# Performance work log

Measured on AMD Instinct MI355X. Metric: run time of the kernel, lower is better.

Reference implementation:

```python
import jax, jax.numpy as jnp
import numpy as np

NEG_SLOPE = 0.2


def gat_conv(x, src, dst, W, a_src, a_dst, bias, heads, out_ch):
    """PyG-style GATConv (concat=True, self-loops already appended)."""
    N = x.shape[0]
    h = (x @ W).reshape(N, heads, out_ch)            # [N,H,C]
    al_s = jnp.einsum('nhc,hc->nh', h, a_src)        # [N,H]
    al_d = jnp.einsum('nhc,hc->nh', h, a_dst)        # [N,H]
    e = al_s[src] + al_d[dst]                        # [E,H]
    e = jnp.where(e > 0, e, NEG_SLOPE * e)           # leaky_relu
    # segment softmax over edges grouped by destination node
    m = jax.ops.segment_max(e, dst, num_segments=N)  # [N,H]
    ex = jnp.exp(e - m[dst])
    s = jax.ops.segment_sum(ex, dst, num_segments=N)
    alpha = ex / s[dst]                              # [E,H]
    msg = alpha[:, :, None] * h[src]                 # [E,H,C]
    out = jax.ops.segment_sum(msg, dst, num_segments=N)  # [N,H,C]
    return out.reshape(N, heads * out_ch) + bias


def setup_inputs() -> dict:
    key = jax.random.key(0)
    ks = jax.random.split(key, 10)
    N, E = 100000, 1600000
    return {
        'x': jax.random.normal(ks[0], (N, 4), dtype=jnp.float32),
        'edge_index': jax.random.randint(ks[1], (2, E), 0, N, dtype=jnp.int64),
        'W1': jax.random.normal(ks[2], (4, 32), dtype=jnp.float32) * 0.5,
        'a_src1': jax.random.normal(ks[3], (2, 16), dtype=jnp.float32) * 0.5,
        'a_dst1': jax.random.normal(ks[4], (2, 16), dtype=jnp.float32) * 0.5,
        'b1': jax.random.normal(ks[5], (32,), dtype=jnp.float32) * 0.1,
        'W2': jax.random.normal(ks[6], (32, 2), dtype=jnp.float32) * 0.2,
        'a_src2': jax.random.normal(ks[7], (1, 2), dtype=jnp.float32) * 0.5,
        'a_dst2': jax.random.normal(ks[8], (1, 2), dtype=jnp.float32) * 0.5,
        'b2': jax.random.normal(ks[9], (2,), dtype=jnp.float32) * 0.1,
    }


def reference(x, edge_index, W1, a_src1, a_dst1, b1, W2, a_src2, a_dst2, b2):
    N = x.shape[0]
    loop = jnp.arange(N, dtype=edge_index.dtype)     # add_self_loops=True
    src = jnp.concatenate([edge_index[0], loop])
    dst = jnp.concatenate([edge_index[1], loop])
    # dropout(p=0.6) is identity at inference
    h = gat_conv(x, src, dst, W1, a_src1, a_dst1, b1, heads=2, out_ch=16)
    h = jax.nn.elu(h)
    out = gat_conv(h, src, dst, W2, a_src2, a_dst2, b2, heads=1, out_ch=2)
    return out
```

## Files before the change

### kernel.cpp

```cpp
#include <hip/hip_runtime.h>
#include <math.h>

#define NEG_SLOPE 0.2f
#define SCAN_CHUNK 2048
#define ECLAMP 80.0f
#define BUCKET_SHIFT 8
#define BUCKET_MASK 255
#define EB_CHUNK 8192

__device__ __forceinline__ float lrelu(float e) {
    return e > 0.f ? e : NEG_SLOPE * e;
}

__global__ void k0_prep1(const float* __restrict__ x,
                         const float* __restrict__ W1,
                         const float* __restrict__ a_src1,
                         const float* __restrict__ a_dst1,
                         float* __restrict__ as1,
                         float* __restrict__ ad1,
                         int N) {
    int t = blockIdx.x * blockDim.x + threadIdx.x;
    int n = t >> 5;
    int c = t & 31;
    if (n >= N) return;
    const float4 xv = reinterpret_cast<const float4*>(x)[n];
    float h = xv.x * W1[c] + xv.y * W1[32 + c] + xv.z * W1[64 + c] + xv.w * W1[96 + c];
    float ts = h * a_src1[c];
    float td = h * a_dst1[c];
#pragma unroll
    for (int m = 8; m >= 1; m >>= 1) {
        ts += __shfl_xor(ts, m);
        td += __shfl_xor(td, m);
    }
    if ((c & 15) == 0) {
        int hh = c >> 4;
        as1[n * 2 + hh] = ts;
        ad1[n * 2 + hh] = td;
    }
}

__global__ void p1_hist(const int* __restrict__ dst, int* __restrict__ cmatT,
                        int E, int NB, int nblkE) {
    __shared__ int cnt[512];
    const int blk = blockIdx.x, tid = threadIdx.x;
    for (int b = tid; b < NB; b += 256) cnt[b] = 0;
    __syncthreads();
    int base = blk * EB_CHUNK;
    int end = min(base + EB_CHUNK, E);
    for (int e = base + tid; e < end; e += 256)
        atomicAdd(&cnt[dst[e] >> BUCKET_SHIFT], 1);
    __syncthreads();
    for (int b = tid; b < NB; b += 256)
        cmatT[(size_t)b * nblkE + blk] = cnt[b];
}

__global__ void k2a_partials(const int* __restrict__ in, int* __restrict__ bsum, int n) {
    __shared__ int ws[4];
    const int tid = threadIdx.x;
    const int lane = tid & 63, wid = tid >> 6;
    int base = blockIdx.x * SCAN_CHUNK + tid * 8;
    int lsum = 0;
#pragma unroll
    for (int i = 0; i < 8; ++i) {
        int idx = base + i;
        lsum += (idx < n) ? in[idx] : 0;
    }
#pragma unroll
    for (int m = 32; m >= 1; m >>= 1) lsum += __shfl_xor(lsum, m);
    if (lane == 0) ws[wid] = lsum;
    __syncthreads();
    if (tid == 0) bsum[blockIdx.x] = ws[0] + ws[1] + ws[2] + ws[3];
}

__global__ void k2b_scanb(const int* __restrict__ bsum, int* __restrict__ bscan, int nb) {
    __shared__ int wsum[16];
    const int tid = threadIdx.x;
    const int lane = tid & 63, wid = tid >> 6;
    int carry = 0;
    for (int base = 0; base < nb; base += 1024) {
        int i = base + tid;
        int v = (i < nb) ? bsum[i] : 0;
        int xx = v;
#pragma unroll
        for (int off = 1; off < 64; off <<= 1) {
            int t = __shfl_up(xx, off);
            if (lane >= off) xx += t;
        }
        if (lane == 63) wsum[wid] = xx;
        __syncthreads();
        int woff = 0;
        for (int w = 0; w < wid; ++w) woff += wsum[w];
        if (i < nb) bscan[i] = carry + woff + xx - v;
        int tot = 0;
        for (int w = 0; w < 16; ++w) tot += wsum[w];
        carry += tot;
        __syncthreads();
    }
}

__global__ void k2c_scan(const int* __restrict__ in, const int* __restrict__ bscan,
                         int* __restrict__ out, int n) {
    __shared__ int ws[4];
    const int tid = threadIdx.x;
    const int lane = tid & 63, wid = tid >> 6;
    int base = blockIdx.x * SCAN_CHUNK + tid * 8;
    int v[8], pre[8];
    int lsum = 0;
#pragma unroll
    for (int i = 0; i < 8; ++i) {
        int idx = base + i;
        v[i] = (idx < n) ? in[idx] : 0;
        pre[i] = lsum;
        lsum += v[i];
    }
    int xs = lsum;
#pragma unroll
    for (int off = 1; off < 64; off <<= 1) {
        int t = __shfl_up(xs, off);
        if (lane >= off) xs += t;
    }
    if (lane == 63) ws[wid] = xs;
    __syncthreads();
    int woff = 0;
    for (int w = 0; w < wid; ++w) woff += ws[w];
    int off0 = bscan[blockIdx.x] + woff + xs - lsum;
#pragma unroll
    for (int i = 0; i < 8; ++i) {
        int idx = base + i;
        if (idx < n) out[idx] = off0 + pre[i];
    }
}

__global__ void p3_scatter(const int* __restrict__ src, const int* __restrict__ dst,
                           const int* __restrict__ cscan, unsigned int* __restrict__ ebuf,
                           int E, int NB, int nblkE) {
    __shared__ int cur[512];
    const int blk = blockIdx.x, tid = threadIdx.x;
    for (int b = tid; b < NB; b += 256)
        cur[b] = cscan[(size_t)b * nblkE + blk];
    __syncthreads();
    int base = blk * EB_CHUNK;
    int end = min(base + EB_CHUNK, E);
    for (int e = base + tid; e < end; e += 256) {
        int d = dst[e];
        int b = d >> BUCKET_SHIFT;
        int pos = atomicAdd(&cur[b], 1);
        ebuf[pos] = (unsigned int)src[e] | ((unsigned int)(d & BUCKET_MASK) << 24);
    }
}

__global__ void p4_csr(const unsigned int* __restrict__ ebuf,
                       const int* __restrict__ cscan,
                       int* __restrict__ rp, int* __restrict__ esrt,
                       int N, int E, int NB, int nblkE) {
    __shared__ int degl[256];
    __shared__ int curl[256];
    __shared__ int wsum[4];
    const int b = blockIdx.x, tid = threadIdx.x;
    const int lane = tid & 63, wid = tid >> 6;
    int bstart = cscan[(size_t)b * nblkE];
    int bend = (b + 1 < NB) ? cscan[(size_t)(b + 1) * nblkE] : E;
    degl[tid] = 0;
    __syncthreads();
    for (int i = bstart + tid; i < bend; i += 256)
        atomicAdd(&degl[ebuf[i] >> 24], 1);
    __syncthreads();
    int v = degl[tid];
    int xs = v;
#pragma unroll
    for (int off = 1; off < 64; off <<= 1) {
        int t = __shfl_up(xs, off);
        if (lane >= off) xs += t;
    }
    if (lane == 63) wsum[wid] = xs;
    __syncthreads();
    int woff = 0;
    for (int w = 0; w < wid; ++w) woff += wsum[w];
    int excl = woff + xs - v;
    int node = (b << BUCKET_SHIFT) + tid;
    if (node < N) rp[node] = bstart + excl;
    curl[tid] = bstart + excl;
    if (b == 0 && tid == 0) rp[N] = E;
    __syncthreads();
    for (int i = bstart + tid; i < bend; i += 256) {
        unsigned int ev = ebuf[i];
        int dl = ev >> 24;
        int pos = atomicAdd(&curl[dl], 1);
        esrt[pos] = (int)(ev & 0x00FFFFFFu);
    }
}

__global__ void k4_layer1(const int* __restrict__ rp, const int* __restrict__ esrt,
                          const float* __restrict__ x, const float* __restrict__ as1,
                          const float* __restrict__ ad1, const float* __restrict__ b1,
                          const float* __restrict__ W1,
                          const float* __restrict__ W2, const float* __restrict__ a_src2,
                          const float* __restrict__ a_dst2,
                          float4* __restrict__ h2p, float* __restrict__ ad2,
                          int N) {
    int t = blockIdx.x * blockDim.x + threadIdx.x;
    int n = t >> 3;
    int l = t & 7;
    if (n >= N) return;
    int h = l >> 2;
    int d = l & 3;
    float ad = ad1[n * 2 + h];
    float es = lrelu(as1[n * 2 + h] + ad);
    float ws = __expf(fminf(es, ECLAMP));
    float g0 = ws * x[(size_t)n * 4 + d], g1 = 0.f, g2 = 0.f, g3 = 0.f;
    float s0 = ws, s1 = 0.f, s2 = 0.f, s3 = 0.f;

    int p0 = rp[n], p1 = rp[n + 1];
    int p = p0;
    for (; p + 3 < p1; p += 4) {
        int sa = esrt[p];
        int sb = esrt[p + 1];
        int sc_ = esrt[p + 2];
        int sd = esrt[p + 3];
        float ea = lrelu(as1[(size_t)sa * 2 + h] + ad);
        float eb = lrelu(as1[(size_t)sb * 2 + h] + ad);
        float ec = lrelu(as1[(size_t)sc_ * 2 + h] + ad);
        float ed = lrelu(as1[(size_t)sd * 2 + h] + ad);
        float xa = x[(size_t)sa * 4 + d];
        float xb = x[(size_t)sb * 4 + d];
        float xc = x[(size_t)sc_ * 4 + d];
        float xd = x[(size_t)sd * 4 + d];
        float wa = __expf(fminf(ea, ECLAMP));
        float wb = __expf(fminf(eb, ECLAMP));
        float wc = __expf(fminf(ec, ECLAMP));
        float wd = __expf(fminf(ed, ECLAMP));
        s0 += wa;  g0 += wa * xa;
        s1 += wb;  g1 += wb * xb;
        s2 += wc;  g2 += wc * xc;
        s3 += wd;  g3 += wd * xd;
    }
    for (; p < p1; ++p) {
        int sa = esrt[p];
        float ea = lrelu(as1[(size_t)sa * 2 + h] + ad);
        float xa = x[(size_t)sa * 4 + d];
        float wa = __expf(fminf(ea, ECLAMP));
        s0 += wa;  g0 += wa * xa;
    }
    float s = (s0 + s1) + (s2 + s3);
    float agg = ((g0 + g1) + (g2 + g3)) / s;

    float a2[2][4];
#pragma unroll
    for (int k = 0; k < 8; ++k)
        a2[k >> 2][k & 3] = __shfl(agg, k, 8);

    float t0 = 0.f, t1 = 0.f;
#pragma unroll
    for (int j = 0; j < 4; ++j) {
        int c = l * 4 + j;
        int hc = c >> 4;
        float o = b1[c]
                + a2[hc][0] * W1[c]
                + a2[hc][1] * W1[32 + c]
                + a2[hc][2] * W1[64 + c]
                + a2[hc][3] * W1[96 + c];
        o = o > 0.f ? o : expm1f(o);
        t0 += o * W2[c * 2 + 0];
        t1 += o * W2[c * 2 + 1];
    }
#pragma unroll
    for (int msk = 1; msk <= 4; msk <<= 1) {
        t0 += __shfl_xor(t0, msk);
        t1 += __shfl_xor(t1, msk);
    }
    if (l == 0) {
        float as2v = t0 * a_src2[0] + t1 * a_src2[1];
        float ad2v = t0 * a_dst2[0] + t1 * a_dst2[1];
        h2p[n] = make_float4(t0, t1, as2v, 0.f);
        ad2[n] = ad2v;
    }
}

__global__ void k5_layer2(const int* __restrict__ rp, const int* __restrict__ esrt,
                          const float4* __restrict__ h2p, const float* __restrict__ ad2,
                          const float* __restrict__ b2,
                          float* __restrict__ out, int N) {
    int t = blockIdx.x * blockDim.x + threadIdx.x;
    int n = t >> 2;
    int sub = t & 3;
    if (n >= N) return;
    float ad = ad2[n];
    float s = 0.f, xx = 0.f, yy = 0.f;
    if (sub == 0) {
        float4 hv = h2p[n];
        float w = __expf(fminf(lrelu(hv.z + ad), ECLAMP));
        s = w; xx = w * hv.x; yy = w * hv.y;
    }
    int p0 = rp[n], p1 = rp[n + 1];
    for (int p = p0 + sub; p < p1; p += 4) {
        int sn = esrt[p];
        float4 hv = h2p[sn];
        float w = __expf(fminf(lrelu(hv.z + ad), ECLAMP));
        s += w; xx += w * hv.x; yy += w * hv.y;
    }
#pragma unroll
    for (int msk = 1; msk <= 2; msk <<= 1) {
        s  += __shfl_xor(s, msk);
        xx += __shfl_xor(xx, msk);
        yy += __shfl_xor(yy, msk);
    }
    if (sub == 0) {
        float2 o;
        o.x = xx / s + b2[0];
        o.y = yy / s + b2[1];
        reinterpret_cast<float2*>(out)[n] = o;
    }
}

extern "C" void kernel_launch(void* const* d_in, const int* in_sizes, int n_in,
                              void* d_out, int out_size, void* d_ws, size_t ws_size,
                              hipStream_t stream) {
    const float* x      = (const float*)d_in[0];
    const int*   ei     = (const int*)d_in[1];
    const float* W1     = (const float*)d_in[2];
    const float* a_src1 = (const float*)d_in[3];
    const float* a_dst1 = (const float*)d_in[4];
    const float* b1     = (const float*)d_in[5];
    const float* W2     = (const float*)d_in[6];
    const float* a_src2 = (const float*)d_in[7];
    const float* a_dst2 = (const float*)d_in[8];
    const float* b2     = (const float*)d_in[9];
    float* out = (float*)d_out;

    const int N = in_sizes[0] / 4;
    const int E = in_sizes[1] / 2;
    const int* srcp = ei;
    const int* dstp = ei + E;

    const int NB    = (N + BUCKET_MASK) >> BUCKET_SHIFT;
    const int nblkE = (E + EB_CHUNK - 1) / EB_CHUNK;
    const int M     = NB * nblkE;
    const int nb2   = (M + SCAN_CHUNK - 1) / SCAN_CHUNK;

    char* w = (char*)d_ws;
    float4* h2p  = (float4*)w;  w += (size_t)N * sizeof(float4);
    float*  as1  = (float*)w;   w += (size_t)N * 2 * sizeof(float);
    float*  ad1  = (float*)w;   w += (size_t)N * 2 * sizeof(float);
    float*  ad2  = (float*)w;   w += (size_t)N * sizeof(float);
    int* rp     = (int*)w;      w += (size_t)(N + 4) * sizeof(int);
    int* cmatT  = (int*)w;      w += (size_t)M * sizeof(int);
    int* cscan  = (int*)w;      w += (size_t)M * sizeof(int);
    int* bsum   = (int*)w;      w += (size_t)(nb2 + 4) * sizeof(int);
    int* bscan  = (int*)w;      w += (size_t)(nb2 + 4) * sizeof(int);
    unsigned int* ebuf = (unsigned int*)w;  w += (size_t)E * sizeof(unsigned int);
    int* esrt   = (int*)w;      w += (size_t)E * sizeof(int);

    const int BT = 256;
    k0_prep1<<<((size_t)N * 32 + BT - 1) / BT, BT, 0, stream>>>(
        x, W1, a_src1, a_dst1, as1, ad1, N);
    p1_hist<<<nblkE, 256, 0, stream>>>(dstp, cmatT, E, NB, nblkE);
    k2a_partials<<<nb2, 256, 0, stream>>>(cmatT, bsum, M);
    k2b_scanb<<<1, 1024, 0, stream>>>(bsum, bscan, nb2);
    k2c_scan<<<nb2, 256, 0, stream>>>(cmatT, bscan, cscan, M);
    p3_scatter<<<nblkE, 256, 0, stream>>>(srcp, dstp, cscan, ebuf, E, NB, nblkE);
    p4_csr<<<NB, 256, 0, stream>>>(ebuf, cscan, rp, esrt, N, E, NB, nblkE);
    k4_layer1<<<((size_t)N * 8 + BT - 1) / BT, BT, 0, stream>>>(
        rp, esrt, x, as1, ad1, b1, W1, W2, a_src2, a_dst2, h2p, ad2, N);
    k5_layer2<<<((size_t)N * 4 + BT - 1) / BT, BT, 0, stream>>>(
        rp, esrt, h2p, ad2, b2, out, N);
}
```

Measured before the change: 179.2 us.

## Shrink CSR buckets, cache bucket edges in LDS, widen layer-2 lanes per node

Buckets drop from 256 to 128 nodes and edge chunks shrink, which gives more blocks for the histogram, scatter and CSR passes. The CSR kernel now keeps up to 3072 bucket edges in shared memory, so its second pass reads them from LDS instead of global memory. Layer 2 uses 8 lanes per node instead of 4 to expose more parallelism on the edge gather. In exchange the bucket-count matrix grows, which makes the scan larger, and the 12KB LDS buffer may reduce occupancy.

```diff
diff --git a/kernel.cpp b/kernel.cpp
--- a/kernel.cpp
+++ b/kernel.cpp
@@ -4,9 +4,12 @@
 #define NEG_SLOPE 0.2f
 #define SCAN_CHUNK 2048
 #define ECLAMP 80.0f
-#define BUCKET_SHIFT 8
-#define BUCKET_MASK 255
-#define EB_CHUNK 8192
+#define BUCKET_SHIFT 7
+#define BUCKET_MASK 127
+#define NPB 128
+#define NBMAX 1024
+#define EB_CHUNK 2048
+#define P4_CAP 3072
 
 __device__ __forceinline__ float lrelu(float e) {
     return e > 0.f ? e : NEG_SLOPE * e;
@@ -41,7 +44,7 @@
 
 __global__ void p1_hist(const int* __restrict__ dst, int* __restrict__ cmatT,
                         int E, int NB, int nblkE) {
-    __shared__ int cnt[512];
+    __shared__ int cnt[NBMAX];
     const int blk = blockIdx.x, tid = threadIdx.x;
     for (int b = tid; b < NB; b += 256) cnt[b] = 0;
     __syncthreads();
@@ -134,7 +137,7 @@
 __global__ void p3_scatter(const int* __restrict__ src, const int* __restrict__ dst,
                            const int* __restrict__ cscan, unsigned int* __restrict__ ebuf,
                            int E, int NB, int nblkE) {
-    __shared__ int cur[512];
+    __shared__ int cur[NBMAX];
     const int blk = blockIdx.x, tid = threadIdx.x;
     for (int b = tid; b < NB; b += 256)
         cur[b] = cscan[(size_t)b * nblkE + blk];
@@ -153,19 +156,24 @@
                        const int* __restrict__ cscan,
                        int* __restrict__ rp, int* __restrict__ esrt,
                        int N, int E, int NB, int nblkE) {
-    __shared__ int degl[256];
-    __shared__ int curl[256];
+    __shared__ unsigned int ecache[P4_CAP];
+    __shared__ int degl[NPB];
+    __shared__ int curl[NPB];
     __shared__ int wsum[4];
     const int b = blockIdx.x, tid = threadIdx.x;
     const int lane = tid & 63, wid = tid >> 6;
     int bstart = cscan[(size_t)b * nblkE];
     int bend = (b + 1 < NB) ? cscan[(size_t)(b + 1) * nblkE] : E;
-    degl[tid] = 0;
-    __syncthreads();
-    for (int i = bstart + tid; i < bend; i += 256)
-        atomicAdd(&degl[ebuf[i] >> 24], 1);
-    __syncthreads();
-    int v = degl[tid];
+    int cnt = bend - bstart;
+    if (tid < NPB) degl[tid] = 0;
+    __syncthreads();
+    for (int i = tid; i < cnt; i += 256) {
+        unsigned int ev = ebuf[bstart + i];
+        if (i < P4_CAP) ecache[i] = ev;
+        atomicAdd(&degl[ev >> 24], 1);
+    }
+    __syncthreads();
+    int v = (tid < NPB) ? degl[tid] : 0;
     int xs = v;
 #pragma unroll
     for (int off = 1; off < 64; off <<= 1) {
@@ -178,12 +186,14 @@
     for (int w = 0; w < wid; ++w) woff += wsum[w];
     int excl = woff + xs - v;
     int node = (b << BUCKET_SHIFT) + tid;
-    if (node < N) rp[node] = bstart + excl;
-    curl[tid] = bstart + excl;
+    if (tid < NPB) {
+        if (node < N) rp[node] = bstart + excl;
+        curl[tid] = bstart + excl;
+    }
     if (b == 0 && tid == 0) rp[N] = E;
     __syncthreads();
-    for (int i = bstart + tid; i < bend; i += 256) {
-        unsigned int ev = ebuf[i];
+    for (int i = tid; i < cnt; i += 256) {
+        unsigned int ev = (i < P4_CAP) ? ecache[i] : ebuf[bstart + i];
         int dl = ev >> 24;
         int pos = atomicAdd(&curl[dl], 1);
         esrt[pos] = (int)(ev & 0x00FFFFFFu);
@@ -281,8 +291,8 @@
                           const float* __restrict__ b2,
                           float* __restrict__ out, int N) {
     int t = blockIdx.x * blockDim.x + threadIdx.x;
-    int n = t >> 2;
-    int sub = t & 3;
+    int n = t >> 3;
+    int sub = t & 7;
     if (n >= N) return;
     float ad = ad2[n];
     float s = 0.f, xx = 0.f, yy = 0.f;
@@ -292,14 +302,14 @@
         s = w; xx = w * hv.x; yy = w * hv.y;
     }
     int p0 = rp[n], p1 = rp[n + 1];
-    for (int p = p0 + sub; p < p1; p += 4) {
+    for (int p = p0 + sub; p < p1; p += 8) {
         int sn = esrt[p];
         float4 hv = h2p[sn];
         float w = __expf(fminf(lrelu(hv.z + ad), ECLAMP));
         s += w; xx += w * hv.x; yy += w * hv.y;
     }
 #pragma unroll
-    for (int msk = 1; msk <= 2; msk <<= 1) {
+    for (int msk = 1; msk <= 4; msk <<= 1) {
         s  += __shfl_xor(s, msk);
         xx += __shfl_xor(xx, msk);
         yy += __shfl_xor(yy, msk);
@@ -361,6 +371,6 @@
     p4_csr<<<NB, 256, 0, stream>>>(ebuf, cscan, rp, esrt, N, E, NB, nblkE);
     k4_layer1<<<((size_t)N * 8 + BT - 1) / BT, BT, 0, stream>>>(
         rp, esrt, x, as1, ad1, b1, W1, W2, a_src2, a_dst2, h2p, ad2, N);
-    k5_layer2<<<((size_t)N * 4 + BT - 1) / BT, BT, 0, stream>>>(
+    k5_layer2<<<((size_t)N * 8 + BT - 1) / BT, BT, 0, stream>>>(
         rp, esrt, h2p, ad2, b2, out, N);
 }
```

New measurement: 182.8 us. 1.02x slower.
